# Performance work log

Hardware: AMD Instinct MI355X
Metric: run time of the kernel (lower is better)

## Reference

```python
import jax, jax.numpy as jnp
import numpy as np

B, T, FEAT, H, E, NT, NH = 64, 256, 188, 512, 1024, 14, 8
HD = E // NH  # head dim = 128


def _gru_dir(x, w_ih, w_hh, b_ih, b_hh):
    # x: [T, B, in]; PyTorch GRU gate order: r, z, n
    xp = jnp.einsum('tbi,gi->tbg', x, w_ih) + b_ih  # [T,B,3H]

    def step(h, xt):
        hp = h @ w_hh.T + b_hh
        r = jax.nn.sigmoid(xt[..., :H] + hp[..., :H])
        z = jax.nn.sigmoid(xt[..., H:2 * H] + hp[..., H:2 * H])
        n = jnp.tanh(xt[..., 2 * H:] + r * hp[..., 2 * H:])
        h = (1 - z) * n + z * h
        return h, h

    h0 = jnp.zeros((x.shape[1], H), x.dtype)
    _, hs = jax.lax.scan(step, h0, xp)
    return hs  # [T,B,H]


def _bigru(x, wf, wb):
    f = _gru_dir(x, *wf)
    b = _gru_dir(x[::-1], *wb)[::-1]
    return jnp.concatenate([f, b], -1)  # [T,B,2H]


def _forward(features, ne_table, g1f, g1b, g2f, g2b, q_w, q_b, k_w, k_b, v_w, v_b,
             out_w, out_b, lin_w, lin_b, crf_start, crf_end, crf_trans, labels):
    nb = features.shape[0]
    x = features.transpose(1, 0, 2)  # [T,B,FEAT]
    enc = _bigru(x, g1f, g1b)        # [T,B,2H]=[T,B,E]
    # NE embedding: arange(14) rows for every batch element -> [S=14, B, 14]
    ne = jnp.broadcast_to(ne_table[:, None, :], (NT, nb, NT))
    # nn.MultiheadAttention with kdim=vdim=NT
    q = (enc @ q_w.T + q_b).reshape(T, nb, NH, HD)
    k = (ne @ k_w.T + k_b).reshape(NT, nb, NH, HD)
    v = (ne @ v_w.T + v_b).reshape(NT, nb, NH, HD)
    scores = jnp.einsum('tbhd,sbhd->bhts', q, k) / jnp.sqrt(jnp.float32(HD))
    attn = jax.nn.softmax(scores, axis=-1)
    ao = jnp.einsum('bhts,sbhd->tbhd', attn, v).reshape(T, nb, E)
    ao = ao @ out_w.T + out_b
    dec_in = jnp.concatenate([enc, ao], -1)   # [T,B,4H]
    dec = _bigru(dec_in, g2f, g2b)            # [T,B,2H]
    dec = dec @ lin_w.T + lin_b               # [T,B,NT]
    dec = dec.transpose(1, 0, 2)              # [B,T,NT]
    # scaled dot product against NE embeddings -> emissions [B,T,NT]
    logits = jnp.einsum('btd,sd->bts', dec, ne_table) / jnp.sqrt(jnp.float32(NT))
    # CRF negative log likelihood, reduction='mean', full mask
    em = jnp.take_along_axis(logits, labels[..., None], axis=2)[..., 0]  # [B,T]
    num = (crf_start[labels[:, 0]] + em.sum(1)
           + crf_trans[labels[:, :-1], labels[:, 1:]].sum(1)
           + crf_end[labels[:, -1]])
    alpha0 = crf_start + logits[:, 0]  # [B,NT]

    def step(a, e_t):
        a = jax.nn.logsumexp(a[:, :, None] + crf_trans[None] + e_t[:, None, :], axis=1)
        return a, None

    alpha, _ = jax.lax.scan(step, alpha0, logits[:, 1:].transpose(1, 0, 2))
    den = jax.nn.logsumexp(alpha + crf_end, axis=1)
    return -(num - den).mean()


def setup_inputs() -> dict:
    key = jax.random.key(0)
    ks = iter(jax.random.split(key, 40))

    def rn(shape, s=0.05):
        return jax.random.normal(next(ks), shape, jnp.float32) * s

    inp = {}
    inp['features'] = jax.random.normal(next(ks), (B, T, FEAT), jnp.float32)
    inp['labels'] = jax.random.randint(next(ks), (B, T), 0, NT)
    inp['ne_table'] = rn((NT, NT), 0.5).at[0].set(0.0)  # padding_idx=0
    for g, fi in (('gru1', FEAT), ('gru2', 4 * H)):
        for d in ('f', 'b'):
            inp[f'{g}_w_ih_{d}'] = rn((3 * H, fi))
            inp[f'{g}_w_hh_{d}'] = rn((3 * H, H))
            inp[f'{g}_b_ih_{d}'] = rn((3 * H,))
            inp[f'{g}_b_hh_{d}'] = rn((3 * H,))
    inp['q_w'] = rn((E, E)); inp['q_b'] = rn((E,))
    inp['k_w'] = rn((E, NT)); inp['k_b'] = rn((E,))
    inp['v_w'] = rn((E, NT)); inp['v_b'] = rn((E,))
    inp['out_w'] = rn((E, E)); inp['out_b'] = rn((E,))
    inp['lin_w'] = rn((NT, 2 * H)); inp['lin_b'] = rn((NT,))
    inp['crf_start'] = rn((NT,), 0.1)
    inp['crf_end'] = rn((NT,), 0.1)
    inp['crf_trans'] = rn((NT, NT), 0.1)
    return inp


def reference(features, labels, ne_table,
              gru1_w_ih_f, gru1_w_hh_f, gru1_b_ih_f, gru1_b_hh_f,
              gru1_w_ih_b, gru1_w_hh_b, gru1_b_ih_b, gru1_b_hh_b,
              gru2_w_ih_f, gru2_w_hh_f, gru2_b_ih_f, gru2_b_hh_f,
              gru2_w_ih_b, gru2_w_hh_b, gru2_b_ih_b, gru2_b_hh_b,
              q_w, q_b, k_w, k_b, v_w, v_b, out_w, out_b,
              lin_w, lin_b, crf_start, crf_end, crf_trans):
    return _forward(features, ne_table,
                    (gru1_w_ih_f, gru1_w_hh_f, gru1_b_ih_f, gru1_b_hh_f),
                    (gru1_w_ih_b, gru1_w_hh_b, gru1_b_ih_b, gru1_b_hh_b),
                    (gru2_w_ih_f, gru2_w_hh_f, gru2_b_ih_f, gru2_b_hh_f),
                    (gru2_w_ih_b, gru2_w_hh_b, gru2_b_ih_b, gru2_b_hh_b),
                    q_w, q_b, k_w, k_b, v_w, v_b, out_w, out_b,
                    lin_w, lin_b, crf_start, crf_end, crf_trans, labels)
```

## Files before the change

### kernel.cpp

```cpp
#include <hip/hip_runtime.h>
#include <hip/hip_bf16.h>
#include <math.h>

typedef __hip_bfloat16 bf16;
typedef __bf16 bf16x8 __attribute__((ext_vector_type(8)));
typedef float  f32x4  __attribute__((ext_vector_type(4)));
typedef unsigned long long u64;

#define T_SEQ 256
#define BATCH 64
#define FEATD 188
#define HID   512
#define EMB   1024
#define NTAG  14
#define G3    1536
#define GRU_NBLK 32
#define FLAG_LAYER (8 * T_SEQ * 16)

__global__ __launch_bounds__(256) void f32_to_bf16(
    const float* __restrict__ src, bf16* __restrict__ dst, int n4)
{
  int i = blockIdx.x * 256 + threadIdx.x;
  if (i >= n4) return;
  float4 v = *(const float4*)(src + (size_t)i * 4);
  bf16 o[4] = {__float2bfloat16(v.x), __float2bfloat16(v.y),
               __float2bfloat16(v.z), __float2bfloat16(v.w)};
  *(ushort4*)(dst + (size_t)i * 4) = *(ushort4*)o;
}

__global__ __launch_bounds__(256) void gemm_mfma(
    const bf16* __restrict__ A1, int lda1,
    const bf16* __restrict__ A2, int lda2, int K1,
    const bf16* __restrict__ W, int ldw,
    const float* __restrict__ bias,
    bf16* __restrict__ C, int ldc,
    int M, int N, int K)
{
  __shared__ __bf16 As[128][40];
  __shared__ __bf16 Bs[128][40];
  const int bm = blockIdx.y * 128;
  const int bn = blockIdx.x * 128;
  const int tid = threadIdx.x;
  const int wave = tid >> 6, lane = tid & 63;
  const int wr = wave >> 1, wc = wave & 1;
  const int lr = lane & 15, lk = (lane >> 4) << 3;
  f32x4 acc[4][4] = {};
  for (int k0 = 0; k0 < K; k0 += 32) {
#pragma unroll
    for (int p = 0; p < 4; ++p) {
      int i = tid + p * 256;
      int row = i >> 3, q = i & 7;
      int kg = k0 + q * 4;
      ushort4 va{0, 0, 0, 0}, vb{0, 0, 0, 0};
      if (kg < K) {
        const bf16* srca = (kg < K1) ? A1 + (size_t)(bm + row) * lda1 + kg
                                     : A2 + (size_t)(bm + row) * lda2 + (kg - K1);
        va = *(const ushort4*)srca;
        vb = *(const ushort4*)(W + (size_t)(bn + row) * ldw + kg);
      }
      *(ushort4*)&As[row][q * 4] = va;
      *(ushort4*)&Bs[row][q * 4] = vb;
    }
    __syncthreads();
    bf16x8 af[4], bf_[4];
#pragma unroll
    for (int i = 0; i < 4; ++i)
      af[i] = *(const bf16x8*)&As[wr * 64 + i * 16 + lr][lk];
#pragma unroll
    for (int j = 0; j < 4; ++j)
      bf_[j] = *(const bf16x8*)&Bs[wc * 64 + j * 16 + lr][lk];
#pragma unroll
    for (int i = 0; i < 4; ++i)
#pragma unroll
      for (int j = 0; j < 4; ++j)
        acc[i][j] = __builtin_amdgcn_mfma_f32_16x16x32_bf16(af[i], bf_[j], acc[i][j], 0, 0, 0);
    __syncthreads();
  }
#pragma unroll
  for (int j = 0; j < 4; ++j) {
    int n = bn + wc * 64 + j * 16 + lr;
    float bv = bias ? bias[n] : 0.f;
#pragma unroll
    for (int i = 0; i < 4; ++i) {
#pragma unroll
      for (int p = 0; p < 4; ++p) {
        int m = bm + wr * 64 + i * 16 + (lane >> 4) * 4 + p;
        C[(size_t)m * ldc + n] = __float2bfloat16(acc[i][j][p] + bv);
      }
    }
  }
}

__global__ __launch_bounds__(256) void transpose_feat(
    const float* __restrict__ f, bf16* __restrict__ xT)
{
  const int idx = blockIdx.x * 256 + threadIdx.x;
  const int total = BATCH * T_SEQ * FEATD;
  if (idx >= total) return;
  const int i = idx % FEATD;
  const int r = idx / FEATD;
  const int b = r / T_SEQ;
  const int t = r % T_SEQ;
  xT[((size_t)t * BATCH + b) * FEATD + i] = __float2bfloat16(f[idx]);
}

__global__ __launch_bounds__(256, 1) void gru_persist(
    const bf16* __restrict__ xp_f, const bf16* __restrict__ xp_b,
    const bf16* __restrict__ whh_f, const bf16* __restrict__ whh_b,
    const float* __restrict__ bhh_f, const float* __restrict__ bhh_b,
    bf16* __restrict__ out, int* __restrict__ flags)
{
  const int blk = blockIdx.x;
  const int dir = blk >> 4;
  const int ct  = blk & 15;
  const bf16* xp   = dir ? xp_b  : xp_f;
  const bf16* whh  = dir ? whh_b : whh_f;
  const float* bhh = dir ? bhh_b : bhh_f;
  const int off = dir ? HID : 0;
  const int tid = threadIdx.x;
  const int wave = tid >> 6, lane = tid & 63;
  const int lr = lane & 15, lkq = lane >> 4;
  int* fl = flags + (size_t)(dir * 4 + wave) * (T_SEQ * 16);

  __shared__ __bf16 Ws[96][520];
  for (int i = tid; i < 96 * 64; i += 256) {
    int r = i >> 6, q = i & 63;
    int grow = (r >> 5) * HID + ct * 32 + (r & 31);
    *(float4*)&Ws[r][q * 8] = *(const float4*)(whh + (size_t)grow * HID + q * 8);
  }
  __syncthreads();

  float bh[3][2];
#pragma unroll
  for (int g = 0; g < 3; ++g)
#pragma unroll
    for (int nf = 0; nf < 2; ++nf)
      bh[g][nf] = bhh[g * HID + ct * 32 + nf * 16 + lr];

  float hp[2][4] = {};

  bf16 xc[3][2][4];
  {
    const int t0 = dir ? (T_SEQ - 1) : 0;
    const size_t xb = (size_t)t0 * BATCH * G3;
#pragma unroll
    for (int p = 0; p < 4; ++p) {
      const size_t xrow = xb + (size_t)(wave * 16 + lkq * 4 + p) * G3;
#pragma unroll
      for (int g = 0; g < 3; ++g)
#pragma unroll
        for (int nf = 0; nf < 2; ++nf)
          xc[g][nf][p] = xp[xrow + g * HID + ct * 32 + nf * 16 + lr];
    }
  }

  for (int s = 0; s < T_SEQ; ++s) {
    const int t = dir ? (T_SEQ - 1 - s) : s;

    f32x4 acc[3][2] = {};
    if (s > 0) {
      int ready = 0;
      do {
        int f = 1;
        if (lane < 16)
          f = __hip_atomic_load(&fl[(s - 1) * 16 + lane],
                                __ATOMIC_RELAXED, __HIP_MEMORY_SCOPE_AGENT);
        ready = __all(f != 0);
        if (!ready) __builtin_amdgcn_s_sleep(1);
      } while (!ready);
      __builtin_amdgcn_sched_barrier(0);
      const int tp = dir ? t + 1 : t - 1;
      const bf16* arow = out + (size_t)tp * BATCH * EMB + off
                         + (size_t)(wave * 16 + lr) * EMB + lkq * 8;
      u64 h0[16], h1[16];
#pragma unroll
      for (int ki = 0; ki < 16; ++ki) {
        h0[ki] = __hip_atomic_load((const u64*)(arow + ki * 32),
                                   __ATOMIC_RELAXED, __HIP_MEMORY_SCOPE_AGENT);
        h1[ki] = __hip_atomic_load((const u64*)(arow + ki * 32 + 4),
                                   __ATOMIC_RELAXED, __HIP_MEMORY_SCOPE_AGENT);
      }
#pragma unroll
      for (int ki = 0; ki < 16; ++ki) {
        union { u64 v[2]; bf16x8 f; } ua;
        ua.v[0] = h0[ki]; ua.v[1] = h1[ki];
#pragma unroll
        for (int g = 0; g < 3; ++g)
#pragma unroll
          for (int nf = 0; nf < 2; ++nf) {
            bf16x8 b = *(const bf16x8*)&Ws[g * 32 + nf * 16 + lr][ki * 32 + lkq * 8];
            acc[g][nf] = __builtin_amdgcn_mfma_f32_16x16x32_bf16(ua.f, b, acc[g][nf], 0, 0, 0);
          }
      }
    }

    const size_t obase = (size_t)t * BATCH * EMB + off;
#pragma unroll
    for (int nf = 0; nf < 2; ++nf) {
      const int c = ct * 32 + nf * 16 + lr;
#pragma unroll
      for (int p = 0; p < 4; ++p) {
        const int m = wave * 16 + lkq * 4 + p;
        float xr = __bfloat162float(xc[0][nf][p]);
        float xz = __bfloat162float(xc[1][nf][p]);
        float xn = __bfloat162float(xc[2][nf][p]);
        float r = 1.f / (1.f + expf(-(xr + acc[0][nf][p] + bh[0][nf])));
        float z = 1.f / (1.f + expf(-(xz + acc[1][nf][p] + bh[1][nf])));
        float n = tanhf(xn + r * (acc[2][nf][p] + bh[2][nf]));
        float h = (1.f - z) * n + z * hp[nf][p];
        hp[nf][p] = h;
        bf16 hvb = __float2bfloat16(h);
        int mb = *(unsigned short*)&hvb;
        int pb = __shfl_xor(mb, 1);
        if (!(lr & 1)) {
          unsigned int pk = (unsigned int)mb | ((unsigned int)pb << 16);
          __hip_atomic_store((unsigned int*)(out + obase + (size_t)m * EMB + c), pk,
                             __ATOMIC_RELAXED, __HIP_MEMORY_SCOPE_AGENT);
        }
      }
    }

    asm volatile("s_waitcnt vmcnt(0)" ::: "memory");
    if (s + 1 < T_SEQ) {
      if (lane == 0)
        __hip_atomic_store(&fl[s * 16 + ct], 1,
                           __ATOMIC_RELAXED, __HIP_MEMORY_SCOPE_AGENT);
      const int tn = dir ? (T_SEQ - 2 - s) : (s + 1);
      const size_t xb2 = (size_t)tn * BATCH * G3;
#pragma unroll
      for (int p = 0; p < 4; ++p) {
        const size_t xrow = xb2 + (size_t)(wave * 16 + lkq * 4 + p) * G3;
#pragma unroll
        for (int g = 0; g < 3; ++g)
#pragma unroll
          for (int nf = 0; nf < 2; ++nf)
            xc[g][nf][p] = xp[xrow + g * HID + ct * 32 + nf * 16 + lr];
      }
    }
  }
}

__global__ __launch_bounds__(256) void kv_kernel(
    const float* __restrict__ ne, const float* __restrict__ k_w,
    const float* __restrict__ k_b, const float* __restrict__ v_w,
    const float* __restrict__ v_b, float* __restrict__ kk,
    float* __restrict__ vv)
{
  const int e = blockIdx.x * 256 + threadIdx.x;
  if (e >= EMB) return;
#pragma unroll
  for (int s = 0; s < NTAG; ++s) {
    float a = k_b[e], c = v_b[e];
#pragma unroll
    for (int i = 0; i < NTAG; ++i) {
      float nv = ne[s * NTAG + i];
      a = fmaf(nv, k_w[e * NTAG + i], a);
      c = fmaf(nv, v_w[e * NTAG + i], c);
    }
    kk[s * EMB + e] = a;
    vv[s * EMB + e] = c;
  }
}

__global__ __launch_bounds__(256) void attn_kernel(
    const bf16* __restrict__ q, const float* __restrict__ kk,
    const float* __restrict__ vv, bf16* __restrict__ ao)
{
  const int unit = blockIdx.x * 4 + (threadIdx.x >> 6);
  const int h = unit & 7;
  const int tb = unit >> 3;
  const int lane = threadIdx.x & 63;
  const size_t qbase = (size_t)tb * EMB + h * 128;
  const int kbase = h * 128 + lane;
  float q0 = __bfloat162float(q[qbase + lane]);
  float q1 = __bfloat162float(q[qbase + 64 + lane]);
  float sc[NTAG];
#pragma unroll
  for (int j = 0; j < NTAG; ++j) {
    float p = q0 * kk[j * EMB + kbase] + q1 * kk[j * EMB + 64 + kbase];
#pragma unroll
    for (int d = 32; d; d >>= 1) p += __shfl_xor(p, d);
    sc[j] = p * 0.088388347648318447f;
  }
  float m = sc[0];
#pragma unroll
  for (int j = 1; j < NTAG; ++j) m = fmaxf(m, sc[j]);
  float sum = 0.f;
#pragma unroll
  for (int j = 0; j < NTAG; ++j) { sc[j] = expf(sc[j] - m); sum += sc[j]; }
  float inv = 1.f / sum;
  float o0 = 0.f, o1 = 0.f;
#pragma unroll
  for (int j = 0; j < NTAG; ++j) {
    float p = sc[j] * inv;
    o0 = fmaf(p, vv[j * EMB + kbase], o0);
    o1 = fmaf(p, vv[j * EMB + 64 + kbase], o1);
  }
  ao[qbase + lane] = __float2bfloat16(o0);
  ao[qbase + 64 + lane] = __float2bfloat16(o1);
}

__global__ __launch_bounds__(256) void dec_logits_kernel(
    const bf16* __restrict__ dec, const float* __restrict__ lin_w,
    const float* __restrict__ lin_b, const float* __restrict__ ne,
    float* __restrict__ logits)
{
  const int tb = blockIdx.x * 4 + (threadIdx.x >> 6);
  const int t = tb >> 6;
  const int b = tb & 63;
  const int lane = threadIdx.x & 63;
  const bf16* drow = dec + (size_t)tb * EMB;
  float dv[16];
#pragma unroll
  for (int i = 0; i < 16; ++i) dv[i] = __bfloat162float(drow[lane + 64 * i]);
  float dl[NTAG];
#pragma unroll
  for (int n = 0; n < NTAG; ++n) {
    float p = 0.f;
#pragma unroll
    for (int i = 0; i < 16; ++i)
      p = fmaf(dv[i], lin_w[n * EMB + lane + 64 * i], p);
#pragma unroll
    for (int d = 32; d; d >>= 1) p += __shfl_xor(p, d);
    dl[n] = p + lin_b[n];
  }
  if (lane < NTAG) {
    float acc = 0.f;
#pragma unroll
    for (int d2 = 0; d2 < NTAG; ++d2)
      acc = fmaf(dl[d2], ne[lane * NTAG + d2], acc);
    logits[((size_t)b * T_SEQ + t) * NTAG + lane] = acc * 0.26726124191242439f;
  }
}

__global__ __launch_bounds__(64) void crf_kernel(
    const float* __restrict__ logits, const int* __restrict__ labels,
    const float* __restrict__ cstart, const float* __restrict__ cend,
    const float* __restrict__ ctrans, float* __restrict__ lossb)
{
  const int b = blockIdx.x;
  const int lane = threadIdx.x;
  __shared__ float al[NTAG];
  __shared__ float tr[NTAG * NTAG];
  __shared__ float tmp[NTAG];
  const float* lg = logits + (size_t)b * T_SEQ * NTAG;
  const int* lab = labels + (size_t)b * T_SEQ;
  for (int i = lane; i < NTAG * NTAG; i += 64) tr[i] = ctrans[i];
  if (lane < NTAG) al[lane] = cstart[lane] + lg[lane];
  __syncthreads();
  for (int t = 1; t < T_SEQ; ++t) {
    float v = 0.f;
    if (lane < NTAG) {
      float mx = -1e30f;
#pragma unroll
      for (int i = 0; i < NTAG; ++i) mx = fmaxf(mx, al[i] + tr[i * NTAG + lane]);
      float sm = 0.f;
#pragma unroll
      for (int i = 0; i < NTAG; ++i) sm += expf(al[i] + tr[i * NTAG + lane] - mx);
      v = mx + logf(sm) + lg[t * NTAG + lane];
    }
    __syncthreads();
    if (lane < NTAG) al[lane] = v;
    __syncthreads();
  }
  float em = 0.f;
  for (int t = lane; t < T_SEQ; t += 64) em += lg[t * NTAG + lab[t]];
  float trs = 0.f;
  for (int t = lane; t < T_SEQ - 1; t += 64) trs += tr[lab[t] * NTAG + lab[t + 1]];
  float p = em + trs;
#pragma unroll
  for (int d = 32; d; d >>= 1) p += __shfl_xor(p, d);
  if (lane < NTAG) tmp[lane] = al[lane] + cend[lane];
  __syncthreads();
  if (lane == 0) {
    float num = p + cstart[lab[0]] + cend[lab[T_SEQ - 1]];
    float mx = tmp[0];
#pragma unroll
    for (int i = 1; i < NTAG; ++i) mx = fmaxf(mx, tmp[i]);
    float sm = 0.f;
#pragma unroll
    for (int i = 0; i < NTAG; ++i) sm += expf(tmp[i] - mx);
    float den = mx + logf(sm);
    lossb[b] = -(num - den);
  }
}

__global__ __launch_bounds__(64) void final_reduce(
    const float* __restrict__ lossb, float* __restrict__ out)
{
  float v = lossb[threadIdx.x];
#pragma unroll
  for (int d = 32; d; d >>= 1) v += __shfl_xor(v, d);
  if (threadIdx.x == 0) out[0] = v * (1.f / 64.f);
}

extern "C" void kernel_launch(void* const* d_in, const int* in_sizes, int n_in,
                              void* d_out, int out_size, void* d_ws, size_t ws_size,
                              hipStream_t stream)
{
  const float* features = (const float*)d_in[0];
  const int*   labels   = (const int*)d_in[1];
  const float* ne_table = (const float*)d_in[2];
  const float* g1_wih_f = (const float*)d_in[3];
  const float* g1_whh_f = (const float*)d_in[4];
  const float* g1_bih_f = (const float*)d_in[5];
  const float* g1_bhh_f = (const float*)d_in[6];
  const float* g1_wih_b = (const float*)d_in[7];
  const float* g1_whh_b = (const float*)d_in[8];
  const float* g1_bih_b = (const float*)d_in[9];
  const float* g1_bhh_b = (const float*)d_in[10];
  const float* g2_wih_f = (const float*)d_in[11];
  const float* g2_whh_f = (const float*)d_in[12];
  const float* g2_bih_f = (const float*)d_in[13];
  const float* g2_bhh_f = (const float*)d_in[14];
  const float* g2_wih_b = (const float*)d_in[15];
  const float* g2_whh_b = (const float*)d_in[16];
  const float* g2_bih_b = (const float*)d_in[17];
  const float* g2_bhh_b = (const float*)d_in[18];
  const float* q_w   = (const float*)d_in[19];
  const float* q_b   = (const float*)d_in[20];
  const float* k_w   = (const float*)d_in[21];
  const float* k_b   = (const float*)d_in[22];
  const float* v_w   = (const float*)d_in[23];
  const float* v_b   = (const float*)d_in[24];
  const float* out_w = (const float*)d_in[25];
  const float* out_b = (const float*)d_in[26];
  const float* lin_w = (const float*)d_in[27];
  const float* lin_b = (const float*)d_in[28];
  const float* crf_start = (const float*)d_in[29];
  const float* crf_end   = (const float*)d_in[30];
  const float* crf_trans = (const float*)d_in[31];

  const size_t NTB = (size_t)T_SEQ * BATCH;
  char* base = (char*)d_ws;
  size_t off = 0;
  auto alloc = [&](size_t bytes) {
    char* p = base + off;
    off += (bytes + 255) & ~(size_t)255;
    return p;
  };
  bf16* xpA  = (bf16*)alloc(NTB * G3 * sizeof(bf16));
  bf16* xpB  = (bf16*)alloc(NTB * G3 * sizeof(bf16));
  bf16* enc  = (bf16*)alloc(NTB * EMB * sizeof(bf16));
  bf16* bufD = (bf16*)alloc(NTB * EMB * sizeof(bf16));
  bf16* bufE = (bf16*)alloc(NTB * EMB * sizeof(bf16));
  float* kkbuf  = (float*)alloc((size_t)NTAG * EMB * sizeof(float));
  float* vvbuf  = (float*)alloc((size_t)NTAG * EMB * sizeof(float));
  float* logits = (float*)alloc(NTB * NTAG * sizeof(float));
  float* lossb  = (float*)alloc(64 * sizeof(float));
  int*   flags  = (int*)alloc(2 * FLAG_LAYER * sizeof(int));
  bf16* w1if = (bf16*)alloc((size_t)G3 * FEATD * sizeof(bf16));
  bf16* w1ib = (bf16*)alloc((size_t)G3 * FEATD * sizeof(bf16));
  bf16* w1hf = (bf16*)alloc((size_t)G3 * HID * sizeof(bf16));
  bf16* w1hb = (bf16*)alloc((size_t)G3 * HID * sizeof(bf16));
  bf16* w2if = (bf16*)alloc((size_t)G3 * 2 * EMB * sizeof(bf16));
  bf16* w2ib = (bf16*)alloc((size_t)G3 * 2 * EMB * sizeof(bf16));
  bf16* w2hf = (bf16*)alloc((size_t)G3 * HID * sizeof(bf16));
  bf16* w2hb = (bf16*)alloc((size_t)G3 * HID * sizeof(bf16));
  bf16* wq   = (bf16*)alloc((size_t)EMB * EMB * sizeof(bf16));
  bf16* wo   = (bf16*)alloc((size_t)EMB * EMB * sizeof(bf16));
  (void)off; (void)ws_size; (void)in_sizes; (void)n_in; (void)out_size;

  bf16* xT = bufD;

  const int M = (int)NTB;
  dim3 blk(256);

  hipMemsetAsync(flags, 0, 2 * FLAG_LAYER * sizeof(int), stream);

  auto conv = [&](const float* s, bf16* d, size_t n) {
    f32_to_bf16<<<(int)((n / 4 + 255) / 256), blk, 0, stream>>>(s, d, (int)(n / 4));
  };
  conv(g1_wih_f, w1if, (size_t)G3 * FEATD);
  conv(g1_wih_b, w1ib, (size_t)G3 * FEATD);
  conv(g1_whh_f, w1hf, (size_t)G3 * HID);
  conv(g1_whh_b, w1hb, (size_t)G3 * HID);
  conv(g2_wih_f, w2if, (size_t)G3 * 2 * EMB);
  conv(g2_wih_b, w2ib, (size_t)G3 * 2 * EMB);
  conv(g2_whh_f, w2hf, (size_t)G3 * HID);
  conv(g2_whh_b, w2hb, (size_t)G3 * HID);
  conv(q_w, wq, (size_t)EMB * EMB);
  conv(out_w, wo, (size_t)EMB * EMB);

  transpose_feat<<<(BATCH * T_SEQ * FEATD + 255) / 256, blk, 0, stream>>>(features, xT);

  dim3 g_xp(G3 / 128, M / 128);
  dim3 g_e(EMB / 128, M / 128);

  gemm_mfma<<<g_xp, blk, 0, stream>>>(xT, FEATD, nullptr, 0, FEATD,
                                      w1if, FEATD, g1_bih_f, xpA, G3, M, G3, FEATD);
  gemm_mfma<<<g_xp, blk, 0, stream>>>(xT, FEATD, nullptr, 0, FEATD,
                                      w1ib, FEATD, g1_bih_b, xpB, G3, M, G3, FEATD);

  gru_persist<<<GRU_NBLK, blk, 0, stream>>>(xpA, xpB, w1hf, w1hb,
                                            g1_bhh_f, g1_bhh_b, enc, flags);

  kv_kernel<<<4, blk, 0, stream>>>(ne_table, k_w, k_b, v_w, v_b, kkbuf, vvbuf);
  gemm_mfma<<<g_e, blk, 0, stream>>>(enc, EMB, nullptr, 0, EMB,
                                     wq, EMB, q_b, bufE, EMB, M, EMB, EMB);

  attn_kernel<<<M * 2, blk, 0, stream>>>(bufE, kkbuf, vvbuf, bufD);
  gemm_mfma<<<g_e, blk, 0, stream>>>(bufD, EMB, nullptr, 0, EMB,
                                     wo, EMB, out_b, bufE, EMB, M, EMB, EMB);

  gemm_mfma<<<g_xp, blk, 0, stream>>>(enc, EMB, bufE, EMB, EMB,
                                      w2if, 2 * EMB, g2_bih_f, xpA, G3, M, G3, 2 * EMB);
  gemm_mfma<<<g_xp, blk, 0, stream>>>(enc, EMB, bufE, EMB, EMB,
                                      w2ib, 2 * EMB, g2_bih_b, xpB, G3, M, G3, 2 * EMB);

  gru_persist<<<GRU_NBLK, blk, 0, stream>>>(xpA, xpB, w2hf, w2hb,
                                            g2_bhh_f, g2_bhh_b, bufD,
                                            flags + FLAG_LAYER);

  dec_logits_kernel<<<M / 4, blk, 0, stream>>>(bufD, lin_w, lin_b, ne_table, logits);

  crf_kernel<<<BATCH, 64, 0, stream>>>(logits, labels, crf_start, crf_end, crf_trans, lossb);
  final_reduce<<<1, 64, 0, stream>>>(lossb, (float*)d_out);
}
```

Measured before the change: 4.604 ms.

## Split persistent GRU recurrence across 64 blocks with 16 columns each

The persistent GRU kernel now uses 32 blocks per direction instead of 16, each owning 16 hidden columns per gate rather than 32. Per-block MFMA work, shared-memory weight footprint and register state are halved, so each timestep's critical path shortens. In exchange, every wave must poll twice as many flags per step, and more blocks must co-reside for the spin-wait scheme to avoid deadlock.

```diff
diff --git a/kernel.cpp b/kernel.cpp
--- a/kernel.cpp
+++ b/kernel.cpp
@@ -14,8 +14,8 @@
 #define EMB   1024
 #define NTAG  14
 #define G3    1536
-#define GRU_NBLK 32
-#define FLAG_LAYER (8 * T_SEQ * 16)
+#define GRU_NBLK 64
+#define FLAG_LAYER (8 * T_SEQ * 32)
 
 __global__ __launch_bounds__(256) void f32_to_bf16(
     const float* __restrict__ src, bf16* __restrict__ dst, int n4)
@@ -111,8 +111,8 @@
     bf16* __restrict__ out, int* __restrict__ flags)
 {
   const int blk = blockIdx.x;
-  const int dir = blk >> 4;
-  const int ct  = blk & 15;
+  const int dir = blk >> 5;
+  const int ct  = blk & 31;
   const bf16* xp   = dir ? xp_b  : xp_f;
   const bf16* whh  = dir ? whh_b : whh_f;
   const float* bhh = dir ? bhh_b : bhh_f;
@@ -120,26 +120,24 @@
   const int tid = threadIdx.x;
   const int wave = tid >> 6, lane = tid & 63;
   const int lr = lane & 15, lkq = lane >> 4;
-  int* fl = flags + (size_t)(dir * 4 + wave) * (T_SEQ * 16);
-
-  __shared__ __bf16 Ws[96][520];
-  for (int i = tid; i < 96 * 64; i += 256) {
+  int* fl = flags + (size_t)(dir * 4 + wave) * (T_SEQ * 32);
+
+  __shared__ __bf16 Ws[48][520];
+  for (int i = tid; i < 48 * 64; i += 256) {
     int r = i >> 6, q = i & 63;
-    int grow = (r >> 5) * HID + ct * 32 + (r & 31);
+    int grow = (r >> 4) * HID + ct * 16 + (r & 15);
     *(float4*)&Ws[r][q * 8] = *(const float4*)(whh + (size_t)grow * HID + q * 8);
   }
   __syncthreads();
 
-  float bh[3][2];
+  float bh[3];
 #pragma unroll
   for (int g = 0; g < 3; ++g)
-#pragma unroll
-    for (int nf = 0; nf < 2; ++nf)
-      bh[g][nf] = bhh[g * HID + ct * 32 + nf * 16 + lr];
-
-  float hp[2][4] = {};
-
-  bf16 xc[3][2][4];
+    bh[g] = bhh[g * HID + ct * 16 + lr];
+
+  float hp[4] = {};
+
+  bf16 xc[3][4];
   {
     const int t0 = dir ? (T_SEQ - 1) : 0;
     const size_t xb = (size_t)t0 * BATCH * G3;
@@ -148,22 +146,20 @@
       const size_t xrow = xb + (size_t)(wave * 16 + lkq * 4 + p) * G3;
 #pragma unroll
       for (int g = 0; g < 3; ++g)
-#pragma unroll
-        for (int nf = 0; nf < 2; ++nf)
-          xc[g][nf][p] = xp[xrow + g * HID + ct * 32 + nf * 16 + lr];
+        xc[g][p] = xp[xrow + g * HID + ct * 16 + lr];
     }
   }
 
   for (int s = 0; s < T_SEQ; ++s) {
     const int t = dir ? (T_SEQ - 1 - s) : s;
 
-    f32x4 acc[3][2] = {};
+    f32x4 acc[3] = {};
     if (s > 0) {
       int ready = 0;
       do {
         int f = 1;
-        if (lane < 16)
-          f = __hip_atomic_load(&fl[(s - 1) * 16 + lane],
+        if (lane < 32)
+          f = __hip_atomic_load(&fl[(s - 1) * 32 + lane],
                                 __ATOMIC_RELAXED, __HIP_MEMORY_SCOPE_AGENT);
         ready = __all(f != 0);
         if (!ready) __builtin_amdgcn_s_sleep(1);
@@ -185,45 +181,40 @@
         union { u64 v[2]; bf16x8 f; } ua;
         ua.v[0] = h0[ki]; ua.v[1] = h1[ki];
 #pragma unroll
-        for (int g = 0; g < 3; ++g)
-#pragma unroll
-          for (int nf = 0; nf < 2; ++nf) {
-            bf16x8 b = *(const bf16x8*)&Ws[g * 32 + nf * 16 + lr][ki * 32 + lkq * 8];
-            acc[g][nf] = __builtin_amdgcn_mfma_f32_16x16x32_bf16(ua.f, b, acc[g][nf], 0, 0, 0);
-          }
+        for (int g = 0; g < 3; ++g) {
+          bf16x8 b = *(const bf16x8*)&Ws[g * 16 + lr][ki * 32 + lkq * 8];
+          acc[g] = __builtin_amdgcn_mfma_f32_16x16x32_bf16(ua.f, b, acc[g], 0, 0, 0);
+        }
       }
     }
 
     const size_t obase = (size_t)t * BATCH * EMB + off;
-#pragma unroll
-    for (int nf = 0; nf < 2; ++nf) {
-      const int c = ct * 32 + nf * 16 + lr;
-#pragma unroll
-      for (int p = 0; p < 4; ++p) {
-        const int m = wave * 16 + lkq * 4 + p;
-        float xr = __bfloat162float(xc[0][nf][p]);
-        float xz = __bfloat162float(xc[1][nf][p]);
-        float xn = __bfloat162float(xc[2][nf][p]);
-        float r = 1.f / (1.f + expf(-(xr + acc[0][nf][p] + bh[0][nf])));
-        float z = 1.f / (1.f + expf(-(xz + acc[1][nf][p] + bh[1][nf])));
-        float n = tanhf(xn + r * (acc[2][nf][p] + bh[2][nf]));
-        float h = (1.f - z) * n + z * hp[nf][p];
-        hp[nf][p] = h;
-        bf16 hvb = __float2bfloat16(h);
-        int mb = *(unsigned short*)&hvb;
-        int pb = __shfl_xor(mb, 1);
-        if (!(lr & 1)) {
-          unsigned int pk = (unsigned int)mb | ((unsigned int)pb << 16);
-          __hip_atomic_store((unsigned int*)(out + obase + (size_t)m * EMB + c), pk,
-                             __ATOMIC_RELAXED, __HIP_MEMORY_SCOPE_AGENT);
-        }
+    const int c = ct * 16 + lr;
+#pragma unroll
+    for (int p = 0; p < 4; ++p) {
+      const int m = wave * 16 + lkq * 4 + p;
+      float xr = __bfloat162float(xc[0][p]);
+      float xz = __bfloat162float(xc[1][p]);
+      float xn = __bfloat162float(xc[2][p]);
+      float r = 1.f / (1.f + expf(-(xr + acc[0][p] + bh[0])));
+      float z = 1.f / (1.f + expf(-(xz + acc[1][p] + bh[1])));
+      float n = tanhf(xn + r * (acc[2][p] + bh[2]));
+      float h = (1.f - z) * n + z * hp[p];
+      hp[p] = h;
+      bf16 hvb = __float2bfloat16(h);
+      int mb = *(unsigned short*)&hvb;
+      int pb = __shfl_xor(mb, 1);
+      if (!(lr & 1)) {
+        unsigned int pk = (unsigned int)mb | ((unsigned int)pb << 16);
+        __hip_atomic_store((unsigned int*)(out + obase + (size_t)m * EMB + c), pk,
+                           __ATOMIC_RELAXED, __HIP_MEMORY_SCOPE_AGENT);
       }
     }
 
     asm volatile("s_waitcnt vmcnt(0)" ::: "memory");
     if (s + 1 < T_SEQ) {
       if (lane == 0)
-        __hip_atomic_store(&fl[s * 16 + ct], 1,
+        __hip_atomic_store(&fl[s * 32 + ct], 1,
                            __ATOMIC_RELAXED, __HIP_MEMORY_SCOPE_AGENT);
       const int tn = dir ? (T_SEQ - 2 - s) : (s + 1);
       const size_t xb2 = (size_t)tn * BATCH * G3;
@@ -232,9 +223,7 @@
         const size_t xrow = xb2 + (size_t)(wave * 16 + lkq * 4 + p) * G3;
 #pragma unroll
         for (int g = 0; g < 3; ++g)
-#pragma unroll
-          for (int nf = 0; nf < 2; ++nf)
-            xc[g][nf][p] = xp[xrow + g * HID + ct * 32 + nf * 16 + lr];
+          xc[g][p] = xp[xrow + g * HID + ct * 16 + lr];
       }
     }
   }
```

Result: faster. 4.301 ms (-6.6%).
